# Optimization experiments

Measured on AMD Instinct MI355X. Metric: run time of the kernel, lower is better.

Reference implementation:

```python
import jax, jax.numpy as jnp
import numpy as np

ALPHA = 0.2          # LeakyReLU negative slope
NEG_INF = -9e15      # mask value from the torch code
B, N, F, E, H, S, T, L = 32, 128, 78, 12, 256, 20, 13, 3


def setup_inputs() -> dict:
    key = jax.random.key(0)
    ks = jax.random.split(key, 20)
    sc = 0.05  # param scale
    inp = {
        "node_features": jax.random.normal(ks[0], (B, N, F), jnp.float32),
        "edge_features": jax.random.normal(ks[1], (B, N, N, E), jnp.float32),
        "adj_matrix": jax.random.randint(ks[2], (B, N, N), 0, 2).astype(jnp.int32),
        "scaffold_features": jax.random.normal(ks[3], (B, S), jnp.float32),
        # node projection (Linear F->H, with bias)
        "W_node": jax.random.normal(ks[4], (F, H), jnp.float32) * sc,
        "b_node": jnp.zeros((H,), jnp.float32),
        # stacked GAT layer params: W (H->H, no bias), a (2H->1, no bias)
        "gat_W": jax.random.normal(ks[5], (L, H, H), jnp.float32) * sc,
        "gat_a": jax.random.normal(ks[6], (L, 2 * H), jnp.float32) * sc,
        # scaffold projection (S->H)
        "W_sc": jax.random.normal(ks[7], (S, H), jnp.float32) * sc,
        "b_sc": jnp.zeros((H,), jnp.float32),
        # graph_pooling MLP: H -> H/2 -> H/4 (shared for graph + scaffold paths)
        "gp_w1": jax.random.normal(ks[8], (H, H // 2), jnp.float32) * sc,
        "gp_b1": jnp.zeros((H // 2,), jnp.float32),
        "gp_w2": jax.random.normal(ks[9], (H // 2, H // 4), jnp.float32) * sc,
        "gp_b2": jnp.zeros((H // 4,), jnp.float32),
        # output MLP: (H/4 + H/4) -> H/2 -> T
        "out_w1": jax.random.normal(ks[10], (H // 2, H // 2), jnp.float32) * sc,
        "out_b1": jnp.zeros((H // 2,), jnp.float32),
        "out_w2": jax.random.normal(ks[11], (H // 2, T), jnp.float32) * sc,
        "out_b2": jnp.zeros((T,), jnp.float32),
    }
    return inp


def _gat_stack(x, adj_matrix, gat_W, gat_a):
    # x: (B,N,H); adj: (B,N,N) int
    mask = adj_matrix > 0
    n_layers, _, h_dim = gat_W.shape
    for l in range(n_layers):
        h = jnp.einsum("bnf,fh->bnh", x, gat_W[l])      # (B,N,H)
        a1, a2 = gat_a[l, :h_dim], gat_a[l, h_dim:]
        # a . [h_i ; h_j] == h_i.a1 + h_j.a2 (exact decomposition of the
        # O(N^2, 2H) concat in the torch code)
        s1 = h @ a1                                       # (B,N)
        s2 = h @ a2                                       # (B,N)
        e = jax.nn.leaky_relu(s1[:, :, None] + s2[:, None, :], ALPHA)
        att = jnp.where(mask, e, NEG_INF)                 # (B,N,N)
        att = jax.nn.softmax(att, axis=-1)
        h_prime = jnp.einsum("bij,bjh->bih", att, h)
        x = jax.nn.relu(h_prime)                          # relu after layer (dropout = identity, eval)
    return x


def _pool(z, gp_w1, gp_b1, gp_w2, gp_b2):
    z = jax.nn.relu(z @ gp_w1 + gp_b1)
    return jax.nn.relu(z @ gp_w2 + gp_b2)


def reference(node_features, edge_features, adj_matrix, scaffold_features,
              W_node, b_node, gat_W, gat_a, W_sc, b_sc,
              gp_w1, gp_b1, gp_w2, gp_b2, out_w1, out_b1, out_w2, out_b2):
    # edge_features is accepted but unused in the original forward
    x = node_features @ W_node + b_node                  # (B,N,H)
    x = _gat_stack(x, adj_matrix, gat_W, gat_a)
    graph = x.mean(axis=1)                               # (B,H)
    g = _pool(graph, gp_w1, gp_b1, gp_w2, gp_b2)         # (B,H/4)
    s = _pool(scaffold_features @ W_sc + b_sc, gp_w1, gp_b1, gp_w2, gp_b2)
    c = jnp.concatenate([g, s], axis=-1)                 # (B,H/2)
    hdn = jax.nn.relu(c @ out_w1 + out_b1)
    return hdn @ out_w2 + out_b2                         # (B,T)
```

## Files before the change

kernel.cpp:

```cpp
#include <hip/hip_runtime.h>
#include <hip/hip_bf16.h>

#define NEG_INF -9.0e15f

using u16 = unsigned short;

__device__ __forceinline__ float b2f(__hip_bfloat16 v) { return __bfloat162float(v); }
__device__ __forceinline__ float ldv(const float* p, int i) { return p[i]; }
__device__ __forceinline__ float ldv(const __hip_bfloat16* p, int i) { return __bfloat162float(p[i]); }

__device__ __forceinline__ void async16(const void* g, void* l) {
    __builtin_amdgcn_global_load_lds(
        (__attribute__((address_space(1))) void*)(g),
        (__attribute__((address_space(3))) void*)(l), 16, 0, 0);
}

__device__ __forceinline__ int sniff(const void* wnode) {
    const u16* w = (const u16*)wnode;
    int lane = threadIdx.x & 63;
    u16 u = w[2 * lane];
    int e = (u >> 7) & 0xFF;
    unsigned long long m = __ballot(e >= 100 && e <= 140);
    return __popcll(m) >= 48;
}

__global__ __launch_bounds__(256) void k_gat(
    const float* __restrict__ x, const void* __restrict__ gat_W,
    const void* __restrict__ gat_a, int layer,
    const void* __restrict__ nf, const void* __restrict__ Wn_raw,
    const void* __restrict__ bn, int first,
    float* __restrict__ h, float* __restrict__ s1, float* __restrict__ s2) {
    __shared__ float xsT[256 * 10];
    const int t = threadIdx.x;
    const int bx = blockIdx.x;
    const int row0 = bx * 8;
    const int tx = t & 63, w = t >> 6;
    const int isbf = sniff(Wn_raw);
    const int c0 = 4 * tx;

    float acc0[4], acc1[4];

    if (isbf) {
        if (first) {
            const u16* nfu = (const u16*)nf;
            for (int i = t; i < 624; i += 256) {
                int r = i / 78, k = i - r * 78;
                xsT[k * 10 + r] = __uint_as_float(((unsigned)nfu[(row0 + r) * 78 + k]) << 16);
            }
            __syncthreads();
            const u16* Wnl = (const u16*)Wn_raw;
            const __hip_bfloat16* bnb = (const __hip_bfloat16*)bn;
            #pragma unroll
            for (int j = 0; j < 4; ++j) { acc0[j] = b2f(bnb[c0 + j]); acc1[j] = acc0[j]; }
            #pragma unroll 2
            for (int k = 0; k < 78; ++k) {
                uint2 wv = *(const uint2*)(Wnl + k * 256 + c0);
                float w0 = __uint_as_float(wv.x << 16);
                float w1 = __uint_as_float(wv.x & 0xffff0000u);
                float w2 = __uint_as_float(wv.y << 16);
                float w3 = __uint_as_float(wv.y & 0xffff0000u);
                float2 xp = *(const float2*)&xsT[k * 10 + 2 * w];
                acc0[0] += xp.x * w0; acc0[1] += xp.x * w1;
                acc0[2] += xp.x * w2; acc0[3] += xp.x * w3;
                acc1[0] += xp.y * w0; acc1[1] += xp.y * w1;
                acc1[2] += xp.y * w2; acc1[3] += xp.y * w3;
            }
            __syncthreads();
            #pragma unroll
            for (int j = 0; j < 4; ++j) {
                xsT[(c0 + j) * 10 + 2 * w]     = acc0[j];
                xsT[(c0 + j) * 10 + 2 * w + 1] = acc1[j];
            }
            __syncthreads();
        } else {
            int r = t >> 5, cb = (t & 31) * 8;
            const float4* xp = (const float4*)(x + (size_t)(row0 + r) * 256 + cb);
            float4 f0 = xp[0], f1 = xp[1];
            xsT[(cb + 0) * 10 + r] = f0.x; xsT[(cb + 1) * 10 + r] = f0.y;
            xsT[(cb + 2) * 10 + r] = f0.z; xsT[(cb + 3) * 10 + r] = f0.w;
            xsT[(cb + 4) * 10 + r] = f1.x; xsT[(cb + 5) * 10 + r] = f1.y;
            xsT[(cb + 6) * 10 + r] = f1.z; xsT[(cb + 7) * 10 + r] = f1.w;
            __syncthreads();
        }
        const u16* Wl = (const u16*)gat_W + (size_t)layer * 65536;
        #pragma unroll
        for (int j = 0; j < 4; ++j) { acc0[j] = 0.f; acc1[j] = 0.f; }
        #pragma unroll 4
        for (int k = 0; k < 256; ++k) {
            uint2 wv = *(const uint2*)(Wl + k * 256 + c0);
            float w0 = __uint_as_float(wv.x << 16);
            float w1 = __uint_as_float(wv.x & 0xffff0000u);
            float w2 = __uint_as_float(wv.y << 16);
            float w3 = __uint_as_float(wv.y & 0xffff0000u);
            float2 xp = *(const float2*)&xsT[k * 10 + 2 * w];
            acc0[0] += xp.x * w0; acc0[1] += xp.x * w1;
            acc0[2] += xp.x * w2; acc0[3] += xp.x * w3;
            acc1[0] += xp.y * w0; acc1[1] += xp.y * w1;
            acc1[2] += xp.y * w2; acc1[3] += xp.y * w3;
        }
        const __hip_bfloat16* ga = (const __hip_bfloat16*)gat_a + (size_t)layer * 512;
        float d10 = 0.f, d20 = 0.f, d11 = 0.f, d21 = 0.f;
        #pragma unroll
        for (int j = 0; j < 4; ++j) {
            float a1v = b2f(ga[c0 + j]), a2v = b2f(ga[256 + c0 + j]);
            d10 += acc0[j] * a1v; d20 += acc0[j] * a2v;
            d11 += acc1[j] * a1v; d21 += acc1[j] * a2v;
        }
        #pragma unroll
        for (int off = 1; off < 64; off <<= 1) {
            d10 += __shfl_xor(d10, off, 64); d20 += __shfl_xor(d20, off, 64);
            d11 += __shfl_xor(d11, off, 64); d21 += __shfl_xor(d21, off, 64);
        }
        if (tx == 0) {
            s1[row0 + 2 * w] = d10;     s2[row0 + 2 * w] = d20;
            s1[row0 + 2 * w + 1] = d11; s2[row0 + 2 * w + 1] = d21;
        }
        *(float4*)&h[(size_t)(row0 + 2 * w) * 256 + c0]     = (float4){acc0[0], acc0[1], acc0[2], acc0[3]};
        *(float4*)&h[(size_t)(row0 + 2 * w + 1) * 256 + c0] = (float4){acc1[0], acc1[1], acc1[2], acc1[3]};
    } else {
        const float* Wlf = (const float*)gat_W + (size_t)layer * 65536;
        const float* gaf = (const float*)gat_a + (size_t)layer * 512;
        if (first) {
            const float* nff = (const float*)nf;
            for (int i = t; i < 624; i += 256) {
                int r = i / 78, k = i - r * 78;
                xsT[k * 10 + r] = nff[(row0 + r) * 78 + k];
            }
            __syncthreads();
            const float* Wnf = (const float*)Wn_raw;
            const float* bnf = (const float*)bn;
            #pragma unroll
            for (int j = 0; j < 4; ++j) { acc0[j] = bnf[c0 + j]; acc1[j] = acc0[j]; }
            for (int k = 0; k < 78; ++k) {
                float4 wf = *(const float4*)(Wnf + k * 256 + c0);
                float2 xp = *(const float2*)&xsT[k * 10 + 2 * w];
                acc0[0] += xp.x * wf.x; acc0[1] += xp.x * wf.y;
                acc0[2] += xp.x * wf.z; acc0[3] += xp.x * wf.w;
                acc1[0] += xp.y * wf.x; acc1[1] += xp.y * wf.y;
                acc1[2] += xp.y * wf.z; acc1[3] += xp.y * wf.w;
            }
            __syncthreads();
            #pragma unroll
            for (int j = 0; j < 4; ++j) {
                xsT[(c0 + j) * 10 + 2 * w]     = acc0[j];
                xsT[(c0 + j) * 10 + 2 * w + 1] = acc1[j];
            }
            __syncthreads();
        } else {
            int r = t >> 5, cb = (t & 31) * 8;
            const float4* xp = (const float4*)(x + (size_t)(row0 + r) * 256 + cb);
            float4 f0 = xp[0], f1 = xp[1];
            xsT[(cb + 0) * 10 + r] = f0.x; xsT[(cb + 1) * 10 + r] = f0.y;
            xsT[(cb + 2) * 10 + r] = f0.z; xsT[(cb + 3) * 10 + r] = f0.w;
            xsT[(cb + 4) * 10 + r] = f1.x; xsT[(cb + 5) * 10 + r] = f1.y;
            xsT[(cb + 6) * 10 + r] = f1.z; xsT[(cb + 7) * 10 + r] = f1.w;
            __syncthreads();
        }
        #pragma unroll
        for (int j = 0; j < 4; ++j) { acc0[j] = 0.f; acc1[j] = 0.f; }
        #pragma unroll 4
        for (int k = 0; k < 256; ++k) {
            float4 wf = *(const float4*)(Wlf + k * 256 + c0);
            float2 xp = *(const float2*)&xsT[k * 10 + 2 * w];
            acc0[0] += xp.x * wf.x; acc0[1] += xp.x * wf.y;
            acc0[2] += xp.x * wf.z; acc0[3] += xp.x * wf.w;
            acc1[0] += xp.y * wf.x; acc1[1] += xp.y * wf.y;
            acc1[2] += xp.y * wf.z; acc1[3] += xp.y * wf.w;
        }
        float d10 = 0.f, d20 = 0.f, d11 = 0.f, d21 = 0.f;
        #pragma unroll
        for (int j = 0; j < 4; ++j) {
            float a1v = gaf[c0 + j], a2v = gaf[256 + c0 + j];
            d10 += acc0[j] * a1v; d20 += acc0[j] * a2v;
            d11 += acc1[j] * a1v; d21 += acc1[j] * a2v;
        }
        #pragma unroll
        for (int off = 1; off < 64; off <<= 1) {
            d10 += __shfl_xor(d10, off, 64); d20 += __shfl_xor(d20, off, 64);
            d11 += __shfl_xor(d11, off, 64); d21 += __shfl_xor(d21, off, 64);
        }
        if (tx == 0) {
            s1[row0 + 2 * w] = d10;     s2[row0 + 2 * w] = d20;
            s1[row0 + 2 * w + 1] = d11; s2[row0 + 2 * w + 1] = d21;
        }
        *(float4*)&h[(size_t)(row0 + 2 * w) * 256 + c0]     = (float4){acc0[0], acc0[1], acc0[2], acc0[3]};
        *(float4*)&h[(size_t)(row0 + 2 * w + 1) * 256 + c0] = (float4){acc1[0], acc1[1], acc1[2], acc1[3]};
    }
}

__global__ __launch_bounds__(256) void k_attn(
    const float* __restrict__ h, const float* __restrict__ s1,
    const float* __restrict__ s2, const int* __restrict__ adj,
    float* __restrict__ x, float* __restrict__ gpart, int do_pool) {
    __shared__ float att_t[128][10];
    __shared__ __align__(16) float hbuf[2][32 * 256];
    __shared__ float pool_red[4][256];
    int blk = blockIdx.x, b = blk >> 4, i0 = (blk & 15) << 3;
    int t = threadIdx.x, w = t >> 6, lane = t & 63;
    const char* hbytes = (const char*)(h + (size_t)b * 32768);
    const int ph = blk & 3;
    {
        char* lb = (char*)&hbuf[0][0];
        const char* g = hbytes + ph * 32768;
        #pragma unroll
        for (int i = 0; i < 8; ++i)
            async16(g + i * 4096 + t * 16, lb + i * 4096 + t * 16);
    }
    {
        int cc0 = lane, cc1 = lane + 64;
        int ir0 = i0 + 2 * w, ir1 = ir0 + 1;
        const int* a0 = adj + (size_t)(b * 128 + ir0) * 128;
        const int* a1 = adj + (size_t)(b * 128 + ir1) * 128;
        int m00 = a0[cc0], m01 = a0[cc1], m10 = a1[cc0], m11 = a1[cc1];
        float sv0 = s1[b * 128 + ir0], sv1 = s1[b * 128 + ir1];
        float t0 = s2[b * 128 + cc0],  t1 = s2[b * 128 + cc1];
        float e00 = sv0 + t0; e00 = (e00 >= 0.f) ? e00 : 0.2f * e00;
        float e01 = sv0 + t1; e01 = (e01 >= 0.f) ? e01 : 0.2f * e01;
        float e10 = sv1 + t0; e10 = (e10 >= 0.f) ? e10 : 0.2f * e10;
        float e11 = sv1 + t1; e11 = (e11 >= 0.f) ? e11 : 0.2f * e11;
        float v00 = (m00 > 0) ? e00 : NEG_INF;
        float v01 = (m01 > 0) ? e01 : NEG_INF;
        float v10 = (m10 > 0) ? e10 : NEG_INF;
        float v11 = (m11 > 0) ? e11 : NEG_INF;
        float mx0 = fmaxf(v00, v01), mx1 = fmaxf(v10, v11);
        #pragma unroll
        for (int off = 1; off < 64; off <<= 1) {
            mx0 = fmaxf(mx0, __shfl_xor(mx0, off, 64));
            mx1 = fmaxf(mx1, __shfl_xor(mx1, off, 64));
        }
        float p00 = __expf(v00 - mx0), p01 = __expf(v01 - mx0);
        float p10 = __expf(v10 - mx1), p11 = __expf(v11 - mx1);
        float s0 = p00 + p01, ss1 = p10 + p11;
        #pragma unroll
        for (int off = 1; off < 64; off <<= 1) {
            s0  += __shfl_xor(s0, off, 64);
            ss1 += __shfl_xor(ss1, off, 64);
        }
        float inv0 = 1.0f / s0, inv1 = 1.0f / ss1;
        att_t[cc0][2 * w]     = p00 * inv0;
        att_t[cc1][2 * w]     = p01 * inv0;
        att_t[cc0][2 * w + 1] = p10 * inv1;
        att_t[cc1][2 * w + 1] = p11 * inv1;
    }
    __syncthreads();
    int tx = t & 63, ty = t >> 6;
    float acc0[4] = {0.f, 0.f, 0.f, 0.f}, acc1[4] = {0.f, 0.f, 0.f, 0.f};
    for (int c = 0; c < 4; ++c) {
        if (c < 3) {
            char* lb = (char*)&hbuf[(c + 1) & 1][0];
            const char* g = hbytes + (((c + 1 + ph) & 3) * 32768);
            #pragma unroll
            for (int i = 0; i < 8; ++i)
                async16(g + i * 4096 + t * 16, lb + i * 4096 + t * 16);
        }
        const float* hc = &hbuf[c & 1][0];
        const int jb = ((c + ph) & 3) * 32;
        #pragma unroll 4
        for (int jj = 0; jj < 32; ++jj) {
            float4 hv = *(const float4*)&hc[jj * 256 + 4 * tx];
            float2 ap = *(const float2*)&att_t[jb + jj][2 * ty];
            acc0[0] += ap.x * hv.x; acc0[1] += ap.x * hv.y;
            acc0[2] += ap.x * hv.z; acc0[3] += ap.x * hv.w;
            acc1[0] += ap.y * hv.x; acc1[1] += ap.y * hv.y;
            acc1[2] += ap.y * hv.z; acc1[3] += ap.y * hv.w;
        }
        __syncthreads();
    }
    if (!do_pool) {
        float4 o0 = {fmaxf(acc0[0],0.f), fmaxf(acc0[1],0.f), fmaxf(acc0[2],0.f), fmaxf(acc0[3],0.f)};
        float4 o1 = {fmaxf(acc1[0],0.f), fmaxf(acc1[1],0.f), fmaxf(acc1[2],0.f), fmaxf(acc1[3],0.f)};
        *(float4*)&x[(size_t)(b * 128 + i0 + 2 * ty)     * 256 + 4 * tx] = o0;
        *(float4*)&x[(size_t)(b * 128 + i0 + 2 * ty + 1) * 256 + 4 * tx] = o1;
    } else {
        float4 pr = {(fmaxf(acc0[0],0.f) + fmaxf(acc1[0],0.f)) * (1.f/128.f),
                     (fmaxf(acc0[1],0.f) + fmaxf(acc1[1],0.f)) * (1.f/128.f),
                     (fmaxf(acc0[2],0.f) + fmaxf(acc1[2],0.f)) * (1.f/128.f),
                     (fmaxf(acc0[3],0.f) + fmaxf(acc1[3],0.f)) * (1.f/128.f)};
        *(float4*)&pool_red[ty][4 * tx] = pr;
        __syncthreads();
        if (t < 64) {
            float4 r0 = ((const float4*)&pool_red[0][0])[t];
            float4 r1 = ((const float4*)&pool_red[1][0])[t];
            float4 r2 = ((const float4*)&pool_red[2][0])[t];
            float4 r3 = ((const float4*)&pool_red[3][0])[t];
            float4 o = {r0.x+r1.x+r2.x+r3.x, r0.y+r1.y+r2.y+r3.y,
                        r0.z+r1.z+r2.z+r3.z, r0.w+r1.w+r2.w+r3.w};
            *(float4*)&gpart[((size_t)b * 16 + (blk & 15)) * 256 + 4 * t] = o;
        }
    }
}

template <typename T>
__device__ __forceinline__ void head_body(
    int b, int t, const float* __restrict__ gpart,
    const T* scaf, const T* W_sc, const T* b_sc,
    const T* gp_w1, const T* gp_b1, const T* gp_w2, const T* gp_b2,
    const T* out_w1, const T* out_b1, const T* out_w2, const T* out_b2,
    float* gin_s, float* sproj, float* scaf_s,
    float* red1, float* red2, float* z1g, float* z1s,
    float* cvec, float* hdn, float* outv) {
    float g = 0.f;
    #pragma unroll
    for (int gg = 0; gg < 16; ++gg) g += gpart[((size_t)b * 16 + gg) * 256 + t];
    gin_s[t] = g;
    if (t < 20) scaf_s[t] = ldv(scaf, b * 20 + t);
    __syncthreads();
    {
        float sa = ldv(b_sc, t);
        #pragma unroll
        for (int k = 0; k < 20; ++k) sa += scaf_s[k] * ldv(W_sc, k * 256 + t);
        sproj[t] = sa;
    }
    __syncthreads();
    {
        int j = t & 127, khalf = t >> 7;
        int k0 = khalf * 128;
        float a1 = 0.f, a2 = 0.f;
        #pragma unroll 16
        for (int kk = 0; kk < 128; ++kk) {
            int k = k0 + kk;
            float wv = ldv(gp_w1, k * 128 + j);
            a1 += gin_s[k] * wv;
            a2 += sproj[k] * wv;
        }
        red1[t] = a1; red2[t] = a2;
    }
    __syncthreads();
    if (t < 128) {
        float bb = ldv(gp_b1, t);
        z1g[t] = fmaxf(bb + red1[t] + red1[t + 128], 0.f);
        z1s[t] = fmaxf(bb + red2[t] + red2[t + 128], 0.f);
    }
    __syncthreads();
    {
        int j = t & 63, q = t >> 6;
        int k0 = q * 32;
        float a1 = 0.f, a2 = 0.f;
        #pragma unroll
        for (int kk = 0; kk < 32; ++kk) {
            int k = k0 + kk;
            float wv = ldv(gp_w2, k * 64 + j);
            a1 += z1g[k] * wv;
            a2 += z1s[k] * wv;
        }
        red1[t] = a1; red2[t] = a2;
    }
    __syncthreads();
    if (t < 64) {
        float bb = ldv(gp_b2, t);
        cvec[t]      = fmaxf(bb + red1[t] + red1[t + 64] + red1[t + 128] + red1[t + 192], 0.f);
        cvec[64 + t] = fmaxf(bb + red2[t] + red2[t + 64] + red2[t + 128] + red2[t + 192], 0.f);
    }
    __syncthreads();
    {
        int j = t & 127, khalf = t >> 7;
        int k0 = khalf * 64;
        float a = 0.f;
        #pragma unroll 16
        for (int kk = 0; kk < 64; ++kk) {
            int k = k0 + kk;
            a += cvec[k] * ldv(out_w1, k * 128 + j);
        }
        red1[t] = a;
    }
    __syncthreads();
    if (t < 128) hdn[t] = fmaxf(ldv(out_b1, t) + red1[t] + red1[t + 128], 0.f);
    __syncthreads();
    if (t < 13) {
        float a = ldv(out_b2, t);
        #pragma unroll 16
        for (int k = 0; k < 128; ++k) a += hdn[k] * ldv(out_w2, k * 13 + t);
        outv[t] = a;
    }
}

__global__ __launch_bounds__(256) void k_head(
    const float* __restrict__ gpart, const void* __restrict__ scaf,
    const void* __restrict__ W_sc, const void* __restrict__ b_sc,
    const void* __restrict__ gp_w1, const void* __restrict__ gp_b1,
    const void* __restrict__ gp_w2, const void* __restrict__ gp_b2,
    const void* __restrict__ out_w1, const void* __restrict__ out_b1,
    const void* __restrict__ out_w2, const void* __restrict__ out_b2,
    void* __restrict__ out, const void* __restrict__ Wn) {
    int isbf = sniff(Wn);
    int b = blockIdx.x;
    int t = threadIdx.x;
    __shared__ float gin_s[256], sproj[256], scaf_s[20];
    __shared__ float red1[256], red2[256];
    __shared__ float z1g[128], z1s[128], cvec[128], hdn[128], outv[13];
    if (isbf) {
        head_body<__hip_bfloat16>(b, t, gpart,
            (const __hip_bfloat16*)scaf, (const __hip_bfloat16*)W_sc, (const __hip_bfloat16*)b_sc,
            (const __hip_bfloat16*)gp_w1, (const __hip_bfloat16*)gp_b1,
            (const __hip_bfloat16*)gp_w2, (const __hip_bfloat16*)gp_b2,
            (const __hip_bfloat16*)out_w1, (const __hip_bfloat16*)out_b1,
            (const __hip_bfloat16*)out_w2, (const __hip_bfloat16*)out_b2,
            gin_s, sproj, scaf_s, red1, red2, z1g, z1s, cvec, hdn, outv);
    } else {
        head_body<float>(b, t, gpart,
            (const float*)scaf, (const float*)W_sc, (const float*)b_sc,
            (const float*)gp_w1, (const float*)gp_b1,
            (const float*)gp_w2, (const float*)gp_b2,
            (const float*)out_w1, (const float*)out_b1,
            (const float*)out_w2, (const float*)out_b2,
            gin_s, sproj, scaf_s, red1, red2, z1g, z1s, cvec, hdn, outv);
    }
    __syncthreads();
    if (t < 13) {
        if (isbf) ((__hip_bfloat16*)out)[b * 13 + t] = __float2bfloat16(outv[t]);
        else      ((float*)out)[b * 13 + t] = outv[t];
    }
}

extern "C" void kernel_launch(void* const* d_in, const int* in_sizes, int n_in,
                              void* d_out, int out_size, void* d_ws, size_t ws_size,
                              hipStream_t stream) {
    (void)in_sizes; (void)n_in; (void)out_size; (void)ws_size;
    const void* nf     = d_in[0];
    const int*  adj    = (const int*)d_in[2];
    const void* scaf   = d_in[3];
    const void* W_node = d_in[4];
    const void* b_node = d_in[5];
    const void* gat_W  = d_in[6];
    const void* gat_a  = d_in[7];
    const void* W_sc   = d_in[8];
    const void* b_sc   = d_in[9];
    const void* gp_w1  = d_in[10];
    const void* gp_b1  = d_in[11];
    const void* gp_w2  = d_in[12];
    const void* gp_b2  = d_in[13];
    const void* out_w1 = d_in[14];
    const void* out_b1 = d_in[15];
    const void* out_w2 = d_in[16];
    const void* out_b2 = d_in[17];

    float* ws    = (float*)d_ws;
    float* x     = ws;
    float* h     = ws + 1048576;
    float* s1    = ws + 2097152;
    float* s2    = s1 + 4096;
    float* gpart = s2 + 4096;

    for (int l = 0; l < 3; ++l) {
        k_gat<<<512, 256, 0, stream>>>(x, gat_W, gat_a, l,
                                       nf, W_node, b_node, (l == 0) ? 1 : 0,
                                       h, s1, s2);
        k_attn<<<512, 256, 0, stream>>>(h, s1, s2, adj, x, gpart, (l == 2) ? 1 : 0);
    }
    k_head<<<32, 256, 0, stream>>>(gpart, scaf, W_sc, b_sc, gp_w1, gp_b1, gp_w2, gp_b2,
                                   out_w1, out_b1, out_w2, out_b2, d_out, W_node);
}
```

Measured before the change: 220.6 us.

## Double-buffer bf16 weight tiles into LDS with async global_load_lds in GAT kernel

```diff
diff --git a/kernel.cpp b/kernel.cpp
--- a/kernel.cpp
+++ b/kernel.cpp
@@ -31,6 +31,7 @@
     const void* __restrict__ bn, int first,
     float* __restrict__ h, float* __restrict__ s1, float* __restrict__ s2) {
     __shared__ float xsT[256 * 10];
+    __shared__ u16 Wbuf[2][32 * 256];
     const int t = threadIdx.x;
     const int bx = blockIdx.x;
     const int row0 = bx * 8;
@@ -41,30 +42,53 @@
     float acc0[4], acc1[4];
 
     if (isbf) {
+        const u16* Wl = (const u16*)gat_W + (size_t)layer * 65536;
+
+        auto stage_rows = [&](const u16* src, int r0, int nr, int b) {
+            const char* g = (const char*)src + (size_t)r0 * 512;
+            char* l = (char*)&Wbuf[b][0];
+            int bytes = nr * 512;
+            for (int off = t * 16; off < bytes; off += 4096)
+                async16(g + off, l + off);
+        };
+        auto tile_compute = [&](int b, int k0, int nr) {
+            const u16* Wb = &Wbuf[b][0];
+            #pragma unroll 8
+            for (int kk = 0; kk < nr; ++kk) {
+                uint2 wv = *(const uint2*)(Wb + kk * 256 + c0);
+                float w0 = __uint_as_float(wv.x << 16);
+                float w1 = __uint_as_float(wv.x & 0xffff0000u);
+                float w2 = __uint_as_float(wv.y << 16);
+                float w3 = __uint_as_float(wv.y & 0xffff0000u);
+                float2 xp = *(const float2*)&xsT[(k0 + kk) * 10 + 2 * w];
+                acc0[0] += xp.x * w0; acc0[1] += xp.x * w1;
+                acc0[2] += xp.x * w2; acc0[3] += xp.x * w3;
+                acc1[0] += xp.y * w0; acc1[1] += xp.y * w1;
+                acc1[2] += xp.y * w2; acc1[3] += xp.y * w3;
+            }
+        };
+
+        int pb;
         if (first) {
+            const u16* Wnl = (const u16*)Wn_raw;
+            stage_rows(Wnl, 0, 32, 0);
             const u16* nfu = (const u16*)nf;
             for (int i = t; i < 624; i += 256) {
                 int r = i / 78, k = i - r * 78;
                 xsT[k * 10 + r] = __uint_as_float(((unsigned)nfu[(row0 + r) * 78 + k]) << 16);
             }
-            __syncthreads();
-            const u16* Wnl = (const u16*)Wn_raw;
             const __hip_bfloat16* bnb = (const __hip_bfloat16*)bn;
             #pragma unroll
             for (int j = 0; j < 4; ++j) { acc0[j] = b2f(bnb[c0 + j]); acc1[j] = acc0[j]; }
-            #pragma unroll 2
-            for (int k = 0; k < 78; ++k) {
-                uint2 wv = *(const uint2*)(Wnl + k * 256 + c0);
-                float w0 = __uint_as_float(wv.x << 16);
-                float w1 = __uint_as_float(wv.x & 0xffff0000u);
-                float w2 = __uint_as_float(wv.y << 16);
-                float w3 = __uint_as_float(wv.y & 0xffff0000u);
-                float2 xp = *(const float2*)&xsT[k * 10 + 2 * w];
-                acc0[0] += xp.x * w0; acc0[1] += xp.x * w1;
-                acc0[2] += xp.x * w2; acc0[3] += xp.x * w3;
-                acc1[0] += xp.y * w0; acc1[1] += xp.y * w1;
-                acc1[2] += xp.y * w2; acc1[3] += xp.y * w3;
-            }
+            __syncthreads();
+            stage_rows(Wnl, 32, 32, 1);
+            tile_compute(0, 0, 32);
+            __syncthreads();
+            stage_rows(Wnl, 64, 14, 0);
+            tile_compute(1, 32, 32);
+            __syncthreads();
+            stage_rows(Wl, 0, 32, 1);
+            tile_compute(0, 64, 14);
             __syncthreads();
             #pragma unroll
             for (int j = 0; j < 4; ++j) {
@@ -72,7 +96,9 @@
                 xsT[(c0 + j) * 10 + 2 * w + 1] = acc1[j];
             }
             __syncthreads();
+            pb = 1;
         } else {
+            stage_rows(Wl, 0, 32, 0);
             int r = t >> 5, cb = (t & 31) * 8;
             const float4* xp = (const float4*)(x + (size_t)(row0 + r) * 256 + cb);
             float4 f0 = xp[0], f1 = xp[1];
@@ -81,22 +107,15 @@
             xsT[(cb + 4) * 10 + r] = f1.x; xsT[(cb + 5) * 10 + r] = f1.y;
             xsT[(cb + 6) * 10 + r] = f1.z; xsT[(cb + 7) * 10 + r] = f1.w;
             __syncthreads();
-        }
-        const u16* Wl = (const u16*)gat_W + (size_t)layer * 65536;
+            pb = 0;
+        }
         #pragma unroll
         for (int j = 0; j < 4; ++j) { acc0[j] = 0.f; acc1[j] = 0.f; }
-        #pragma unroll 4
-        for (int k = 0; k < 256; ++k) {
-            uint2 wv = *(const uint2*)(Wl + k * 256 + c0);
-            float w0 = __uint_as_float(wv.x << 16);
-            float w1 = __uint_as_float(wv.x & 0xffff0000u);
-            float w2 = __uint_as_float(wv.y << 16);
-            float w3 = __uint_as_float(wv.y & 0xffff0000u);
-            float2 xp = *(const float2*)&xsT[k * 10 + 2 * w];
-            acc0[0] += xp.x * w0; acc0[1] += xp.x * w1;
-            acc0[2] += xp.x * w2; acc0[3] += xp.x * w3;
-            acc1[0] += xp.y * w0; acc1[1] += xp.y * w1;
-            acc1[2] += xp.y * w2; acc1[3] += xp.y * w3;
+        for (int tt = 0; tt < 8; ++tt) {
+            if (tt < 7) stage_rows(Wl, 32 * (tt + 1), 32, pb ^ 1);
+            tile_compute(pb, 32 * tt, 32);
+            __syncthreads();
+            pb ^= 1;
         }
         const __hip_bfloat16* ga = (const __hip_bfloat16*)gat_a + (size_t)layer * 512;
         float d10 = 0.f, d20 = 0.f, d11 = 0.f, d21 = 0.f;
```

After: 223.9 us. Within noise of the previous version (+1.5%).
